# Optimization experiments

Measured on AMD Instinct MI355X. Metric: run time of the kernel, lower is better.

The kernel has to match this reference:

```python
import jax, jax.numpy as jnp
import numpy as np

DIM = 1024
HEADS = 16
B, N = 2, 2048


def setup_inputs() -> dict:
    key = jax.random.key(0)
    ks = jax.random.split(key, 10)
    s = 1.0 / np.sqrt(DIM)
    return {
        "y2_for": jax.random.normal(ks[0], (B, N, DIM), jnp.float32),
        "y2_back": jax.random.normal(ks[1], (B, N, DIM), jnp.float32),
        "Wq": jax.random.normal(ks[2], (DIM, DIM), jnp.float32) * s,
        "bq": jnp.zeros((DIM,), jnp.float32),
        "Wk": jax.random.normal(ks[3], (DIM, DIM), jnp.float32) * s,
        "bk": jnp.zeros((DIM,), jnp.float32),
        "Wv": jax.random.normal(ks[4], (DIM, DIM), jnp.float32) * s,
        "bv": jnp.zeros((DIM,), jnp.float32),
        "Wo": jax.random.normal(ks[5], (DIM, DIM), jnp.float32) * s,
        "bo": jnp.zeros((DIM,), jnp.float32),
    }


def reference(y2_for, y2_back, Wq, bq, Wk, bk, Wv, bv, Wo, bo):
    h = HEADS
    d = DIM // h
    scale = d ** -0.5
    q = y2_for @ Wq + bq                    # [b, n, dim]
    k = y2_back @ Wk + bk
    v = (y2_back + y2_for) @ Wv + bv

    def split_heads(x):
        b, n, _ = x.shape
        return x.reshape(b, n, h, d).transpose(0, 2, 1, 3)  # [b, h, n, d]

    q, k, v = split_heads(q), split_heads(k), split_heads(v)
    attn = jax.nn.softmax(jnp.einsum('bhid,bhjd->bhij', q, k) * scale, axis=-1)
    out = jnp.einsum('bhij,bhjd->bhid', attn, v)
    out = out.transpose(0, 2, 1, 3).reshape(y2_for.shape)   # [b, n, dim]
    out = out + y2_for + y2_back
    return out @ Wo + bo
```

## Files before the change

kernel.cpp:

```cpp
#include <hip/hip_runtime.h>

#define DIM 1024
#define HEADS 16
#define BB 2
#define NN 2048
#define HD 64
#define M_ROWS (BB*NN)

typedef __bf16 bf16x8 __attribute__((ext_vector_type(8)));
typedef float f32x4 __attribute__((ext_vector_type(4)));
typedef short s16x4 __attribute__((ext_vector_type(4)));

__device__ inline unsigned short f2bf(float f) {
    unsigned int u = __builtin_bit_cast(unsigned int, f);
    u += 0x7fffu + ((u >> 16) & 1u);
    return (unsigned short)(u >> 16);
}
__device__ inline float bf2f(unsigned short u) {
    return __builtin_bit_cast(float, (unsigned int)u << 16);
}
__device__ inline bf16x8 as_bf16x8(uint4 v) {
    return __builtin_bit_cast(bf16x8, v);
}
__device__ __forceinline__ void gl_lds16(const unsigned short* g, unsigned short* l) {
    __builtin_amdgcn_global_load_lds(
        (const __attribute__((address_space(1))) unsigned int*)g,
        (__attribute__((address_space(3))) unsigned int*)l, 16, 0, 0);
}

__device__ __forceinline__ f32x4 mfma16x16x16bf16(s16x4 a, s16x4 b, f32x4 c) {
#if __has_builtin(__builtin_amdgcn_mfma_f32_16x16x16bf16_1k)
    return __builtin_amdgcn_mfma_f32_16x16x16bf16_1k(a, b, c, 0, 0, 0);
#else
    asm volatile("v_mfma_f32_16x16x16_bf16 %0, %1, %2, %0"
                 : "+v"(c) : "v"(a), "v"(b));
    return c;
#endif
}

__global__ __launch_bounds__(256) void prep_w(
    const float* __restrict__ Wq, const float* __restrict__ Wk,
    const float* __restrict__ Wv, const float* __restrict__ Wo,
    unsigned short* __restrict__ Wt_all)
{
    __shared__ float tile[32][33];
    const int m = blockIdx.z;
    const float* W = (m == 0) ? Wq : (m == 1) ? Wk : (m == 2) ? Wv : Wo;
    const int bk = blockIdx.x, bn = blockIdx.y;
    const int tx = threadIdx.x & 31, ty = threadIdx.x >> 5;

    #pragma unroll
    for (int i = 0; i < 32; i += 8)
        tile[ty + i][tx] = W[(size_t)(bk*32 + ty + i)*DIM + bn*32 + tx];
    __syncthreads();
    unsigned short* dst = Wt_all + (size_t)m * DIM * DIM;
    #pragma unroll
    for (int i = 0; i < 32; i += 8)
        dst[(size_t)(bn*32 + ty + i)*DIM + bk*32 + tx] = f2bf(tile[tx][ty + i]);
}

__global__ __launch_bounds__(256) void prep_act(
    const float* __restrict__ y2f, const float* __restrict__ y2b,
    unsigned short* __restrict__ Af, unsigned short* __restrict__ Ab,
    unsigned short* __restrict__ As)
{
    const size_t idx = ((size_t)blockIdx.x*256 + threadIdx.x) * 8;
    #pragma unroll
    for (int half = 0; half < 2; half++) {
        float4 f = *(const float4*)(y2f + idx + half*4);
        float4 b = *(const float4*)(y2b + idx + half*4);
        ushort4 of, ob, os;
        of.x = f2bf(f.x); of.y = f2bf(f.y); of.z = f2bf(f.z); of.w = f2bf(f.w);
        ob.x = f2bf(b.x); ob.y = f2bf(b.y); ob.z = f2bf(b.z); ob.w = f2bf(b.w);
        os.x = f2bf(f.x + b.x); os.y = f2bf(f.y + b.y);
        os.z = f2bf(f.z + b.z); os.w = f2bf(f.w + b.w);
        *(ushort4*)(Af + idx + half*4) = of;
        *(ushort4*)(Ab + idx + half*4) = ob;
        *(ushort4*)(As + idx + half*4) = os;
    }
}

__global__ __launch_bounds__(256) void gemm_qkv(
    const unsigned short* __restrict__ Af, const unsigned short* __restrict__ Ab,
    const unsigned short* __restrict__ As,
    const unsigned short* __restrict__ Wt_all,
    const float* __restrict__ bq, const float* __restrict__ bk,
    const float* __restrict__ bv,
    unsigned short* __restrict__ Qh, unsigned short* __restrict__ Kh,
    unsigned short* __restrict__ Vt)
{
    const int bm = blockIdx.x;
    const int mode = blockIdx.y >> 3;
    const int bn = blockIdx.y & 7;
    __shared__ __align__(16) unsigned short sA[128*32];
    __shared__ __align__(16) unsigned short sB[128*32];
    const int t = threadIdx.x;
    const int w = t >> 6, lane = t & 63, ln = lane & 15, quad = lane >> 4;
    const int wm = w >> 1, wn = w & 1;
    const unsigned short* Wt = Wt_all + (size_t)mode * (DIM*DIM);
    const unsigned short* A0 = (mode == 0) ? Af : (mode == 1) ? Ab : As;

    const int srow = lane >> 2;
    const int scol = (lane & 3) * 8;

    f32x4 acc[4][4];
    #pragma unroll
    for (int mi = 0; mi < 4; mi++)
        #pragma unroll
        for (int ni = 0; ni < 4; ni++)
            acc[mi][ni] = (f32x4){0.f, 0.f, 0.f, 0.f};

    for (int kt = 0; kt < 32; kt++) {
        __syncthreads();
        #pragma unroll
        for (int j = 0; j < 2; j++) {
            int row = w*32 + j*16;
            gl_lds16(A0 + (size_t)(bm*128 + row + srow)*DIM + kt*32 + scol,
                     &sA[row*32]);
            gl_lds16(Wt + (size_t)(bn*128 + row + srow)*DIM + kt*32 + scol,
                     &sB[row*32]);
        }
        __syncthreads();

        bf16x8 af[4], bfr[4];
        #pragma unroll
        for (int mi = 0; mi < 4; mi++)
            af[mi] = as_bf16x8(*(const uint4*)(&sA[(wm*64 + mi*16 + ln)*32 + quad*8]));
        #pragma unroll
        for (int ni = 0; ni < 4; ni++)
            bfr[ni] = as_bf16x8(*(const uint4*)(&sB[(wn*64 + ni*16 + ln)*32 + quad*8]));
        #pragma unroll
        for (int mi = 0; mi < 4; mi++)
            #pragma unroll
            for (int ni = 0; ni < 4; ni++)
                acc[mi][ni] = __builtin_amdgcn_mfma_f32_16x16x32_bf16(af[mi], bfr[ni], acc[mi][ni], 0, 0, 0);
    }

    const float* bias = (mode == 0) ? bq : (mode == 1) ? bk : bv;
    unsigned short* dst = (mode == 0) ? Qh : (mode == 1) ? Kh : Vt;
    const float sc = (mode == 0) ? 0.125f * 1.4426950408889634f : 1.0f;
    #pragma unroll
    for (int mi = 0; mi < 4; mi++) {
        #pragma unroll
        for (int r = 0; r < 4; r++) {
            int grow = bm*128 + wm*64 + mi*16 + quad*4 + r;
            int b_ = grow >> 11, n = grow & (NN - 1);
            #pragma unroll
            for (int ni = 0; ni < 4; ni++) {
                int gcol = bn*128 + wn*64 + ni*16 + ln;
                int hh = gcol >> 6, dd = gcol & 63;
                float val = (acc[mi][ni][r] + bias[gcol]) * sc;
                if (mode == 2)
                    dst[(((size_t)(b_*HEADS + hh))*HD + dd)*NN + n] = f2bf(val);
                else
                    dst[(((size_t)(b_*HEADS + hh))*NN + n)*HD + dd] = f2bf(val);
            }
        }
    }
}

__global__ __launch_bounds__(256) void gemm_out(
    const unsigned short* __restrict__ attp,
    const unsigned short* __restrict__ Wt_all,
    const float* __restrict__ bo, float* __restrict__ out)
{
    const int bm = blockIdx.x, bn = blockIdx.y;
    __shared__ __align__(16) unsigned short sA[64*32];
    __shared__ __align__(16) unsigned short sB[128*32];
    const int t = threadIdx.x;
    const int w = t >> 6, lane = t & 63, ln = lane & 15, quad = lane >> 4;
    const int wm = w >> 1, wn = w & 1;
    const unsigned short* Wt = Wt_all + (size_t)3 * (DIM*DIM);

    const int srow = lane >> 2;
    const int scol = (lane & 3) * 8;

    f32x4 acc[2][4];
    #pragma unroll
    for (int mi = 0; mi < 2; mi++)
        #pragma unroll
        for (int ni = 0; ni < 4; ni++)
            acc[mi][ni] = (f32x4){0.f, 0.f, 0.f, 0.f};

    for (int kt = 0; kt < 32; kt++) {
        __syncthreads();
        gl_lds16(attp + (size_t)(bm*64 + w*16 + srow)*DIM + kt*32 + scol,
                 &sA[(w*16)*32]);
        #pragma unroll
        for (int j = 0; j < 2; j++) {
            int row = w*32 + j*16;
            gl_lds16(Wt + (size_t)(bn*128 + row + srow)*DIM + kt*32 + scol,
                     &sB[row*32]);
        }
        __syncthreads();

        bf16x8 af[2], bfr[4];
        #pragma unroll
        for (int mi = 0; mi < 2; mi++)
            af[mi] = as_bf16x8(*(const uint4*)(&sA[(wm*32 + mi*16 + ln)*32 + quad*8]));
        #pragma unroll
        for (int ni = 0; ni < 4; ni++)
            bfr[ni] = as_bf16x8(*(const uint4*)(&sB[(wn*64 + ni*16 + ln)*32 + quad*8]));
        #pragma unroll
        for (int mi = 0; mi < 2; mi++)
            #pragma unroll
            for (int ni = 0; ni < 4; ni++)
                acc[mi][ni] = __builtin_amdgcn_mfma_f32_16x16x32_bf16(af[mi], bfr[ni], acc[mi][ni], 0, 0, 0);
    }

    #pragma unroll
    for (int mi = 0; mi < 2; mi++) {
        #pragma unroll
        for (int r = 0; r < 4; r++) {
            int grow = bm*64 + wm*32 + mi*16 + quad*4 + r;
            #pragma unroll
            for (int ni = 0; ni < 4; ni++) {
                int gcol = bn*128 + wn*64 + ni*16 + ln;
                out[(size_t)grow*DIM + gcol] = acc[mi][ni][r] + bo[gcol];
            }
        }
    }
}

__global__ __launch_bounds__(256) void attn_kernel(
    const unsigned short* __restrict__ Qh, const unsigned short* __restrict__ Kh,
    const unsigned short* __restrict__ Vt, const unsigned short* __restrict__ As,
    unsigned short* __restrict__ attp)
{
    const int bh = blockIdx.x;
    const int qt = blockIdx.y;
    const int b = bh >> 4, h = bh & 15;
    const int t = threadIdx.x;
    const int w = t >> 6, lane = t & 63, ln = lane & 15, quad = lane >> 4;
    const int sw = ln & 7;
    const float EBIAS = 17.312340490667562f;

    __shared__ __align__(16) unsigned short sQ[64*64];
    __shared__ __align__(16) unsigned short sK[64*64];
    __shared__ __align__(16) unsigned short sVt[64*64];

    const unsigned short* Qb  = Qh + (size_t)bh * NN * HD + (size_t)qt * 64 * HD;
    const unsigned short* Kb  = Kh + (size_t)bh * NN * HD;
    const unsigned short* Vtb = Vt + (size_t)bh * HD * NN;

    const int rl = lane >> 3, cb = lane & 7;

    #pragma unroll
    for (int j = 0; j < 2; j++) {
        int row = w*16 + j*8 + rl;
        gl_lds16(Qb + (size_t)row*HD + ((cb ^ (row & 7))*8), &sQ[(w*16 + j*8)*64]);
    }
    __syncthreads();
    bf16x8 aq[2];
    #pragma unroll
    for (int k = 0; k < 2; k++)
        aq[k] = as_bf16x8(*(const uint4*)(&sQ[(w*16 + ln)*64 + (((k*4 + quad) ^ sw)*8)]));

    const s16x4 ones = { (short)0x3F80, (short)0x3F80, (short)0x3F80, (short)0x3F80 };
    f32x4 accO[4], accL;
    accL = (f32x4){0.f, 0.f, 0.f, 0.f};
    #pragma unroll
    for (int di = 0; di < 4; di++) accO[di] = (f32x4){0.f, 0.f, 0.f, 0.f};

    for (int jt = 0; jt < 32; jt++) {
        __syncthreads();
        #pragma unroll
        for (int j = 0; j < 2; j++) {
            int row = w*16 + j*8 + rl;
            gl_lds16(Kb + (size_t)(jt*64 + row)*HD + ((cb ^ (row & 7))*8),
                     &sK[(w*16 + j*8)*64]);
            gl_lds16(Vtb + (size_t)row*NN + jt*64 + ((cb ^ (row & 7))*8),
                     &sVt[(w*16 + j*8)*64]);
        }
        __syncthreads();

        f32x4 accS[4];
        #pragma unroll
        for (int ni = 0; ni < 4; ni++) accS[ni] = (f32x4){0.f, 0.f, 0.f, 0.f};
        #pragma unroll
        for (int ni = 0; ni < 4; ni++)
            #pragma unroll
            for (int k = 0; k < 2; k++) {
                bf16x8 bk = as_bf16x8(*(const uint4*)(
                    &sK[(ni*16 + ln)*64 + (((k*4 + quad) ^ sw)*8)]));
                accS[ni] = __builtin_amdgcn_mfma_f32_16x16x32_bf16(bk, aq[k], accS[ni], 0, 0, 0);
            }

        s16x4 pf[4];
        #pragma unroll
        for (int ni = 0; ni < 4; ni++) {
            unsigned int e0 = __builtin_bit_cast(unsigned int, __builtin_amdgcn_exp2f(accS[ni][0] - EBIAS));
            unsigned int e1 = __builtin_bit_cast(unsigned int, __builtin_amdgcn_exp2f(accS[ni][1] - EBIAS));
            unsigned int e2 = __builtin_bit_cast(unsigned int, __builtin_amdgcn_exp2f(accS[ni][2] - EBIAS));
            unsigned int e3 = __builtin_bit_cast(unsigned int, __builtin_amdgcn_exp2f(accS[ni][3] - EBIAS));
            unsigned int lo = __builtin_amdgcn_perm(e1, e0, 0x07060302u);
            unsigned int hi = __builtin_amdgcn_perm(e3, e2, 0x07060302u);
            pf[ni] = __builtin_bit_cast(s16x4, uint2{lo, hi});
            accL = mfma16x16x16bf16(pf[ni], ones, accL);
        }

        #pragma unroll
        for (int ni = 0; ni < 4; ni++) {
            int blkv = 2*ni + (quad >> 1);
            int off = (quad & 1) * 4;
            #pragma unroll
            for (int di = 0; di < 4; di++) {
                s16x4 bv = __builtin_bit_cast(s16x4,
                    *(const uint2*)(&sVt[(di*16 + ln)*64 + ((blkv ^ sw)*8) + off]));
                accO[di] = mfma16x16x16bf16(pf[ni], bv, accO[di]);
            }
        }
    }

    #pragma unroll
    for (int r = 0; r < 4; r++) {
        float inv = 1.f / accL[r];
        int n = qt*64 + w*16 + quad*4 + r;
        #pragma unroll
        for (int di = 0; di < 4; di++) {
            int c = h*64 + di*16 + ln;
            size_t gi = ((size_t)b*NN + n)*DIM + c;
            float o = accO[di][r]*inv + bf2f(As[gi]);
            attp[gi] = f2bf(o);
        }
    }
}

extern "C" void kernel_launch(void* const* d_in, const int* in_sizes, int n_in,
                              void* d_out, int out_size, void* d_ws, size_t ws_size,
                              hipStream_t stream) {
    const float* y2f = (const float*)d_in[0];
    const float* y2b = (const float*)d_in[1];
    const float* Wq  = (const float*)d_in[2];
    const float* bq  = (const float*)d_in[3];
    const float* Wk  = (const float*)d_in[4];
    const float* bk  = (const float*)d_in[5];
    const float* Wv  = (const float*)d_in[6];
    const float* bv  = (const float*)d_in[7];
    const float* Wo  = (const float*)d_in[8];
    const float* bo  = (const float*)d_in[9];
    float* out = (float*)d_out;

    const size_t NACT = (size_t)M_ROWS * DIM;
    unsigned short* ws   = (unsigned short*)d_ws;
    unsigned short* Af   = ws;
    unsigned short* Ab   = ws + NACT;
    unsigned short* As   = ws + 2*NACT;
    unsigned short* Qh   = ws + 3*NACT;
    unsigned short* Kh   = ws + 4*NACT;
    unsigned short* Vt   = ws + 5*NACT;
    unsigned short* Wt   = ws + 6*NACT;
    unsigned short* attp = Ab;

    prep_w<<<dim3(32, 32, 4), 256, 0, stream>>>(Wq, Wk, Wv, Wo, Wt);
    prep_act<<<dim3(2048), 256, 0, stream>>>(y2f, y2b, Af, Ab, As);
    gemm_qkv<<<dim3(32, 24), 256, 0, stream>>>(
        Af, Ab, As, Wt, bq, bk, bv, Qh, Kh, Vt);
    attn_kernel<<<dim3(32, 32), 256, 0, stream>>>(Qh, Kh, Vt, As, attp);
    gemm_out<<<dim3(64, 8), 256, 0, stream>>>(attp, Wt, bo, out);
}
```

Baseline: 226.4 us.

## Double-buffer K/V tiles in attention and coalesce V-transpose stores via LDS

The attention kernel now double-buffers K and V^T tiles in LDS, prefetching the next tile with async global-to-LDS loads while computing the current one, using manual vmcnt waits and raw barriers. Q is loaded directly from global into registers instead of through LDS, and the softmax bias is folded into the accumulator initial value. MFMA sections get raised wave priority. In the QKV GEMM, the transposed V output is staged through shared memory so global writes become coalesced 16-byte stores instead of strided 2-byte scatters. The cost is higher LDS use per block and reliance on exact waitcnt accounting.

New measurement: 242.8 us. 1.07x slower.

```diff
diff --git a/kernel.cpp b/kernel.cpp
--- a/kernel.cpp
+++ b/kernel.cpp
@@ -92,8 +92,9 @@
     const int bm = blockIdx.x;
     const int mode = blockIdx.y >> 3;
     const int bn = blockIdx.y & 7;
-    __shared__ __align__(16) unsigned short sA[128*32];
-    __shared__ __align__(16) unsigned short sB[128*32];
+    __shared__ __align__(16) unsigned short smem[8192];
+    unsigned short* sA = smem;
+    unsigned short* sB = smem + 4096;
     const int t = threadIdx.x;
     const int w = t >> 6, lane = t & 63, ln = lane & 15, quad = lane >> 4;
     const int wm = w >> 1, wn = w & 1;
@@ -138,22 +139,50 @@
 
     const float* bias = (mode == 0) ? bq : (mode == 1) ? bk : bv;
     unsigned short* dst = (mode == 0) ? Qh : (mode == 1) ? Kh : Vt;
-    const float sc = (mode == 0) ? 0.125f * 1.4426950408889634f : 1.0f;
-    #pragma unroll
-    for (int mi = 0; mi < 4; mi++) {
-        #pragma unroll
-        for (int r = 0; r < 4; r++) {
-            int grow = bm*128 + wm*64 + mi*16 + quad*4 + r;
-            int b_ = grow >> 11, n = grow & (NN - 1);
-            #pragma unroll
-            for (int ni = 0; ni < 4; ni++) {
-                int gcol = bn*128 + wn*64 + ni*16 + ln;
-                int hh = gcol >> 6, dd = gcol & 63;
-                float val = (acc[mi][ni][r] + bias[gcol]) * sc;
-                if (mode == 2)
-                    dst[(((size_t)(b_*HEADS + hh))*HD + dd)*NN + n] = f2bf(val);
-                else
+    if (mode < 2) {
+        const float sc = (mode == 0) ? 0.125f * 1.4426950408889634f : 1.0f;
+        #pragma unroll
+        for (int mi = 0; mi < 4; mi++) {
+            #pragma unroll
+            for (int r = 0; r < 4; r++) {
+                int grow = bm*128 + wm*64 + mi*16 + quad*4 + r;
+                int b_ = grow >> 11, n = grow & (NN - 1);
+                #pragma unroll
+                for (int ni = 0; ni < 4; ni++) {
+                    int gcol = bn*128 + wn*64 + ni*16 + ln;
+                    int hh = gcol >> 6, dd = gcol & 63;
+                    float val = (acc[mi][ni][r] + bias[gcol]) * sc;
                     dst[(((size_t)(b_*HEADS + hh))*NN + n)*HD + dd] = f2bf(val);
+                }
+            }
+        }
+    } else {
+        #pragma unroll
+        for (int p = 0; p < 2; p++) {
+            __syncthreads();
+            if (wn == p) {
+                #pragma unroll
+                for (int mi = 0; mi < 4; mi++)
+                    #pragma unroll
+                    for (int ni = 0; ni < 4; ni++) {
+                        float bsv = bias[bn*128 + wn*64 + ni*16 + ln];
+                        ushort4 pk;
+                        pk.x = f2bf(acc[mi][ni][0] + bsv);
+                        pk.y = f2bf(acc[mi][ni][1] + bsv);
+                        pk.z = f2bf(acc[mi][ni][2] + bsv);
+                        pk.w = f2bf(acc[mi][ni][3] + bsv);
+                        *(ushort4*)(&smem[(ni*16 + ln)*128 + wm*64 + mi*16 + quad*4]) = pk;
+                    }
+            }
+            __syncthreads();
+            const int hh = bn*2 + p, b_ = bm >> 4;
+            unsigned short* vrow = dst + (((size_t)(b_*HEADS + hh))*HD)*NN
+                                       + (size_t)(bm & 15)*128;
+            #pragma unroll
+            for (int i = 0; i < 4; i++) {
+                int idx = i*256 + t;
+                int dd = idx >> 4, ch = (idx & 15)*8;
+                *(uint4*)(vrow + (size_t)dd*NN + ch) = *(const uint4*)(&smem[dd*128 + ch]);
             }
         }
     }
@@ -235,9 +264,8 @@
     const int sw = ln & 7;
     const float EBIAS = 17.312340490667562f;
 
-    __shared__ __align__(16) unsigned short sQ[64*64];
-    __shared__ __align__(16) unsigned short sK[64*64];
-    __shared__ __align__(16) unsigned short sVt[64*64];
+    __shared__ __align__(16) unsigned short sK[2][64*64];
+    __shared__ __align__(16) unsigned short sVt[2][64*64];
 
     const unsigned short* Qb  = Qh + (size_t)bh * NN * HD + (size_t)qt * 64 * HD;
     const unsigned short* Kb  = Kh + (size_t)bh * NN * HD;
@@ -245,16 +273,20 @@
 
     const int rl = lane >> 3, cb = lane & 7;
 
-    #pragma unroll
-    for (int j = 0; j < 2; j++) {
-        int row = w*16 + j*8 + rl;
-        gl_lds16(Qb + (size_t)row*HD + ((cb ^ (row & 7))*8), &sQ[(w*16 + j*8)*64]);
-    }
-    __syncthreads();
     bf16x8 aq[2];
     #pragma unroll
     for (int k = 0; k < 2; k++)
-        aq[k] = as_bf16x8(*(const uint4*)(&sQ[(w*16 + ln)*64 + (((k*4 + quad) ^ sw)*8)]));
+        aq[k] = as_bf16x8(*(const uint4*)(Qb + (size_t)(w*16 + ln)*HD + (k*4 + quad)*8));
+
+#define STAGE_KV(JT, BBUF) do { \
+        _Pragma("unroll") \
+        for (int j = 0; j < 2; j++) { \
+            int row = w*16 + j*8 + rl; \
+            gl_lds16(Kb + (size_t)((JT)*64 + row)*HD + ((cb ^ (row & 7))*8), \
+                     &sK[BBUF][(w*16 + j*8)*64]); \
+            gl_lds16(Vtb + (size_t)row*NN + (JT)*64 + ((cb ^ (row & 7))*8), \
+                     &sVt[BBUF][(w*16 + j*8)*64]); \
+        } } while (0)
 
     const s16x4 ones = { (short)0x3F80, (short)0x3F80, (short)0x3F80, (short)0x3F80 };
     f32x4 accO[4], accL;
@@ -262,43 +294,52 @@
     #pragma unroll
     for (int di = 0; di < 4; di++) accO[di] = (f32x4){0.f, 0.f, 0.f, 0.f};
 
+    STAGE_KV(0, 0);
+
+    #pragma unroll 2
     for (int jt = 0; jt < 32; jt++) {
-        __syncthreads();
-        #pragma unroll
-        for (int j = 0; j < 2; j++) {
-            int row = w*16 + j*8 + rl;
-            gl_lds16(Kb + (size_t)(jt*64 + row)*HD + ((cb ^ (row & 7))*8),
-                     &sK[(w*16 + j*8)*64]);
-            gl_lds16(Vtb + (size_t)row*NN + jt*64 + ((cb ^ (row & 7))*8),
-                     &sVt[(w*16 + j*8)*64]);
-        }
-        __syncthreads();
+        const int cur = jt & 1;
+        if (jt < 31) {
+            STAGE_KV(jt + 1, cur ^ 1);
+            asm volatile("s_waitcnt vmcnt(4)" ::: "memory");
+        } else {
+            asm volatile("s_waitcnt vmcnt(0)" ::: "memory");
+        }
+        __builtin_amdgcn_s_barrier();
+        __builtin_amdgcn_sched_barrier(0);
+
+        const unsigned short* sKc = sK[cur];
+        const unsigned short* sVc = sVt[cur];
 
         f32x4 accS[4];
         #pragma unroll
-        for (int ni = 0; ni < 4; ni++) accS[ni] = (f32x4){0.f, 0.f, 0.f, 0.f};
+        for (int ni = 0; ni < 4; ni++)
+            accS[ni] = (f32x4){-EBIAS, -EBIAS, -EBIAS, -EBIAS};
+        __builtin_amdgcn_s_setprio(1);
         #pragma unroll
         for (int ni = 0; ni < 4; ni++)
             #pragma unroll
             for (int k = 0; k < 2; k++) {
-                bf16x8 bk = as_bf16x8(*(const uint4*)(
-                    &sK[(ni*16 + ln)*64 + (((k*4 + quad) ^ sw)*8)]));
-                accS[ni] = __builtin_amdgcn_mfma_f32_16x16x32_bf16(bk, aq[k], accS[ni], 0, 0, 0);
-            }
+                bf16x8 bkf = as_bf16x8(*(const uint4*)(
+                    &sKc[(ni*16 + ln)*64 + (((k*4 + quad) ^ sw)*8)]));
+                accS[ni] = __builtin_amdgcn_mfma_f32_16x16x32_bf16(bkf, aq[k], accS[ni], 0, 0, 0);
+            }
+        __builtin_amdgcn_s_setprio(0);
 
         s16x4 pf[4];
         #pragma unroll
         for (int ni = 0; ni < 4; ni++) {
-            unsigned int e0 = __builtin_bit_cast(unsigned int, __builtin_amdgcn_exp2f(accS[ni][0] - EBIAS));
-            unsigned int e1 = __builtin_bit_cast(unsigned int, __builtin_amdgcn_exp2f(accS[ni][1] - EBIAS));
-            unsigned int e2 = __builtin_bit_cast(unsigned int, __builtin_amdgcn_exp2f(accS[ni][2] - EBIAS));
-            unsigned int e3 = __builtin_bit_cast(unsigned int, __builtin_amdgcn_exp2f(accS[ni][3] - EBIAS));
+            unsigned int e0 = __builtin_bit_cast(unsigned int, __builtin_amdgcn_exp2f(accS[ni][0]));
+            unsigned int e1 = __builtin_bit_cast(unsigned int, __builtin_amdgcn_exp2f(accS[ni][1]));
+            unsigned int e2 = __builtin_bit_cast(unsigned int, __builtin_amdgcn_exp2f(accS[ni][2]));
+            unsigned int e3 = __builtin_bit_cast(unsigned int, __builtin_amdgcn_exp2f(accS[ni][3]));
             unsigned int lo = __builtin_amdgcn_perm(e1, e0, 0x07060302u);
             unsigned int hi = __builtin_amdgcn_perm(e3, e2, 0x07060302u);
             pf[ni] = __builtin_bit_cast(s16x4, uint2{lo, hi});
             accL = mfma16x16x16bf16(pf[ni], ones, accL);
         }
 
+        __builtin_amdgcn_s_setprio(1);
         #pragma unroll
         for (int ni = 0; ni < 4; ni++) {
             int blkv = 2*ni + (quad >> 1);
@@ -306,11 +347,16 @@
             #pragma unroll
             for (int di = 0; di < 4; di++) {
                 s16x4 bv = __builtin_bit_cast(s16x4,
-                    *(const uint2*)(&sVt[(di*16 + ln)*64 + ((blkv ^ sw)*8) + off]));
+                    *(const uint2*)(&sVc[(di*16 + ln)*64 + ((blkv ^ sw)*8) + off]));
                 accO[di] = mfma16x16x16bf16(pf[ni], bv, accO[di]);
             }
         }
-    }
+        __builtin_amdgcn_s_setprio(0);
+
+        __builtin_amdgcn_sched_barrier(0);
+        __builtin_amdgcn_s_barrier();
+    }
+#undef STAGE_KV
 
     #pragma unroll
     for (int r = 0; r < 4; r++) {
```
